# Kernel optimization log

Hardware: AMD Instinct MI355X
Metric: run time of the kernel (lower is better)

## Reference

```python
import jax, jax.numpy as jnp
import numpy as np

AUX_LOSS_COEFF = 0.03125  # config.aux_loss_coeff


def setup_inputs() -> dict:
    key = jax.random.key(0)
    k0, k1 = jax.random.split(key, 2)
    B, T, d, m = 2, 2048, 2048, 16384
    activations = jax.random.normal(k0, (B, T, d), dtype=jnp.float32)
    # kaiming-uniform-ish init, then unit-norm rows (as in _initialize_weights)
    W_enc = jax.random.normal(k1, (m, d), dtype=jnp.float32)
    W_enc = W_enc / (jnp.linalg.norm(W_enc, axis=1, keepdims=True) + 1e-8)
    b_enc = jnp.zeros((m,), dtype=jnp.float32)
    W_emb = W_enc.T  # tied init: W_emb.weight = W_enc.weight.T, shape [d, m]
    steps_since_active = jnp.zeros((m,), dtype=jnp.int32)  # buffer, starts at 0
    return {
        "activations": activations,
        "W_enc": W_enc,
        "b_enc": b_enc,
        "W_emb": W_emb,
        "steps_since_active": steps_since_active,
        "topk": 64,
        "dead_window": 1000,
    }


def reference(activations, W_enc, b_enc, W_emb, steps_since_active, topk, dead_window):
    B, T, d = activations.shape
    m = W_enc.shape[0]
    # pre_act = W_enc(activations)  -> [B, T, m]
    pre_act = jnp.einsum("btd,md->btm", activations, W_enc) + b_enc
    # top-k over concept dim
    top_vals, top_idx = jax.lax.top_k(pre_act, topk)  # [B, T, k]
    # sparse = zeros scatter top_vals at top_idx along last dim
    flat_idx = top_idx.reshape(-1, topk)   # [B*T, k]
    flat_vals = top_vals.reshape(-1, topk)
    rows = jnp.arange(flat_idx.shape[0])[:, None]
    sparse = (
        jnp.zeros((flat_idx.shape[0], m), dtype=pre_act.dtype)
        .at[rows, flat_idx]
        .set(flat_vals)
        .reshape(B, T, m)
    )
    # encoded = W_emb(sparse) -> [B, T, d]
    encoded = jnp.einsum("btm,dm->btd", sparse, W_emb)
    # aux loss on dead concepts (dead_mask all False at init -> 0.0)
    dead_mask = (steps_since_active >= dead_window).astype(pre_act.dtype)  # [m]
    n_dead = jnp.sum(dead_mask)
    denom = jnp.maximum(n_dead * B * T, 1.0)
    dead_mean = jnp.sum(pre_act * dead_mask) / denom
    aux_loss = jnp.where(n_dead > 0, -dead_mean * AUX_LOSS_COEFF, jnp.zeros((), pre_act.dtype))
    return encoded, aux_loss
```

## Files before the change

kernel.cpp:

```cpp
#include <hip/hip_runtime.h>
#include <cfloat>
#include <climits>


typedef __attribute__((ext_vector_type(8))) short short8;
typedef __attribute__((ext_vector_type(4))) float f32x4;

#define NC      96
#define KFIN    64
#define TAU     1e-3f
#define AUXC    0.03125f
#define MCONC   16384
#define DDIM    2048
#define CAP     768

__device__ __forceinline__ ushort f2bf(float f) {
  unsigned u = __float_as_uint(f);
  u += 0x7fff + ((u >> 16) & 1);
  return (ushort)(u >> 16);
}
__device__ __forceinline__ float bf2f(ushort h) {
  return __uint_as_float(((unsigned)h) << 16);
}

__global__ void k_init(float* dead_sum, int* n_dead, int* wl_count) {
  *dead_sum = 0.f;
  *n_dead = 0;
  *wl_count = 0;
}

__global__ void k_count_dead(const int* __restrict__ steps, const int* __restrict__ dw,
                             int m, int* __restrict__ n_dead) {
  int i = blockIdx.x * blockDim.x + threadIdx.x;
  if (i < m && steps[i] >= *dw) atomicAdd(n_dead, 1);
}

__global__ void k_final(const float* __restrict__ ds, const int* __restrict__ nd,
                        float* __restrict__ outp, float BT) {
  int n = *nd;
  float denom = fmaxf((float)n * BT, 1.0f);
  outp[0] = (n > 0) ? -((*ds) / denom) * AUXC : 0.0f;
}

__global__ __launch_bounds__(256)
void k_stage2(const float* __restrict__ srcA, ushort* __restrict__ dstA, int totA,
              const float* __restrict__ srcB, ushort* __restrict__ dstB, int totB,
              int K) {
  int idx = blockIdx.x * 256 + threadIdx.x;
  const float* src;
  ushort* dst;
  int t;
  if (idx < totA) { src = srcA; dst = dstA; t = idx; }
  else if (idx < totA + totB) { src = srcB; dst = dstB; t = idx - totA; }
  else return;
  int nch = K >> 5;
  int row = t / nch, c = t - row * nch;
  const float* s = src + (size_t)row * K + c * 32;
  float f[32];
#pragma unroll
  for (int q = 0; q < 8; ++q) *(float4*)&f[q * 4] = *(const float4*)(s + q * 4);
  ushort hi[32];
  float lof[32];
#pragma unroll
  for (int e = 0; e < 32; ++e) {
    hi[e] = f2bf(f[e]);
    lof[e] = f[e] - bf2f(hi[e]);
  }
  ushort* d = dst + (size_t)row * ((size_t)K * 2) + c * 64;
#pragma unroll
  for (int q = 0; q < 4; ++q) {
    short8 o;
#pragma unroll
    for (int e = 0; e < 8; ++e) o[e] = (short)hi[q * 8 + e];
    *(short8*)(d + q * 8) = o;
  }
#pragma unroll
  for (int q = 0; q < 4; ++q) {
    short8 o;
#pragma unroll
    for (int e = 0; e < 8; ++e) o[e] = (short)f2bf(lof[q * 8 + e]);
    *(short8*)(d + 32 + q * 8) = o;
  }
}

__device__ __forceinline__ void gload16(const void* g, void* l) {
  __builtin_amdgcn_global_load_lds((const __attribute__((address_space(1))) void*)g,
                                   (__attribute__((address_space(3))) void*)l, 16, 0, 0);
}

__global__ __launch_bounds__(256, 3)
void k_gemm3(const ushort* __restrict__ Ast, const ushort* __restrict__ Bst,
             const float* __restrict__ bias, float* __restrict__ C,
             int row0, int K, int m, int nbm) {
  __shared__ ushort As[128 * 64];
  __shared__ ushort Bs[128 * 64];
  const int tid = threadIdx.x;
  const int lane = tid & 63, w = tid >> 6;
  const int wm = w >> 1, wn = w & 1;

  const int nbn = m >> 7;
  const int nwg = nbm * nbn;
  const int q = nwg >> 3, r = nwg & 7;
  const int x = blockIdx.x & 7, i0 = blockIdx.x >> 3;
  const int wg = (x < r) ? x * (q + 1) + i0 : r * (q + 1) + (x - r) * q + i0;
  const int bm = wg / nbn, bn = wg % nbn;

  const size_t K2 = (size_t)K * 2;
  const int nch = K >> 5;

  const int gr = lane >> 3;
  const int swz = (((lane & 7) ^ gr) << 3);
  const size_t arow0 = (size_t)(row0 + bm * 128);
  const size_t brow0 = (size_t)(bn * 128);

  f32x4 acc[4][4];
#pragma unroll
  for (int i = 0; i < 4; ++i)
#pragma unroll
    for (int j = 0; j < 4; ++j) acc[i][j] = (f32x4)(0.f);

  const int kg = lane >> 4;
  const int j7 = lane & 7;
  const int sh = ((kg ^ j7) << 3);
  const int rbase = (lane & 15) * 64;

  for (int c = 0; c < nch; ++c) {
#pragma unroll
    for (int t = 0; t < 4; ++t) {
      int i = w * 4 + t;
      int rr = i * 8 + gr;
      gload16(Ast + (arow0 + rr) * K2 + (size_t)c * 64 + swz, (void*)(As + i * 512));
      gload16(Bst + (brow0 + rr) * K2 + (size_t)c * 64 + swz, (void*)(Bs + i * 512));
    }
    __syncthreads();
    short8 ah[4], al[4], bh[4], bl[4];
#pragma unroll
    for (int f = 0; f < 4; ++f) {
      const ushort* pa = As + (wm * 64 + f * 16) * 64 + rbase;
      ah[f] = *(const short8*)(pa + sh);
      al[f] = *(const short8*)(pa + (sh ^ 32));
      const ushort* pb = Bs + (wn * 64 + f * 16) * 64 + rbase;
      bh[f] = *(const short8*)(pb + sh);
      bl[f] = *(const short8*)(pb + (sh ^ 32));
    }
#pragma unroll
    for (int fm = 0; fm < 4; ++fm)
#pragma unroll
      for (int fn = 0; fn < 4; ++fn) {
        acc[fm][fn] = __builtin_amdgcn_mfma_f32_16x16x32_bf16(ah[fm], bh[fn], acc[fm][fn], 0, 0, 0);
        acc[fm][fn] = __builtin_amdgcn_mfma_f32_16x16x32_bf16(ah[fm], bl[fn], acc[fm][fn], 0, 0, 0);
        acc[fm][fn] = __builtin_amdgcn_mfma_f32_16x16x32_bf16(al[fm], bh[fn], acc[fm][fn], 0, 0, 0);
      }
    __syncthreads();
  }

  const int orow = bm * 128 + wm * 64;
  const int ocol = bn * 128 + wn * 64;
#pragma unroll
  for (int fn = 0; fn < 4; ++fn) {
    float bb = bias[ocol + fn * 16 + (lane & 15)];
#pragma unroll
    for (int fm = 0; fm < 4; ++fm) {
      int rb = orow + fm * 16 + (lane >> 4) * 4;
#pragma unroll
      for (int rr = 0; rr < 4; ++rr)
        __builtin_nontemporal_store(acc[fm][fn][rr] + bb,
            &C[(size_t)(rb + rr) * m + ocol + fn * 16 + (lane & 15)]);
    }
  }
}

__global__ __launch_bounds__(256)
void k_topk(const float* __restrict__ preact, int row0,
            const int* __restrict__ steps, const int* __restrict__ dw,
            const int* __restrict__ topk_d,
            float* __restrict__ cvals, int* __restrict__ cidx,
            float* __restrict__ dead_sum,
            int* __restrict__ rowflag, int* __restrict__ wl, int* __restrict__ wl_count,
            float* __restrict__ tvals, int* __restrict__ tidx) {
  __shared__ float dred[4];
  __shared__ float wmx[4], wmn[4];
  __shared__ int scnt;
  __shared__ int pos;
  __shared__ float cval_s[CAP];
  __shared__ int cidx_s[CAP];
  __shared__ float vk1_s, vk_s;
  __shared__ int flag_s;
  const int tid = threadIdx.x;
  const int lane = tid & 63;
  const int grow = row0 + blockIdx.x;
  const float* pr = preact + (size_t)blockIdx.x * MCONC;

  int kt = *topk_d;
  if (kt > KFIN) kt = KFIN;
  if (kt < 1) kt = 1;

  float v[64];
#pragma unroll
  for (int c = 0; c < 16; ++c) {
    const f32x4* p4 = (const f32x4*)(pr + (size_t)c * 1024 + tid * 4);
    f32x4 t4 = __builtin_nontemporal_load(p4);
    v[c * 4 + 0] = t4[0]; v[c * 4 + 1] = t4[1];
    v[c * 4 + 2] = t4[2]; v[c * 4 + 3] = t4[3];
  }

  int dwv = *dw;
  float ds = 0.f;
#pragma unroll
  for (int c = 0; c < 16; ++c) {
    int4 st = *(const int4*)(steps + c * 1024 + tid * 4);
    if (st.x >= dwv) ds += v[c * 4 + 0];
    if (st.y >= dwv) ds += v[c * 4 + 1];
    if (st.z >= dwv) ds += v[c * 4 + 2];
    if (st.w >= dwv) ds += v[c * 4 + 3];
  }
  for (int off = 32; off; off >>= 1) ds += __shfl_down(ds, off);
  if (lane == 0) dred[tid >> 6] = ds;

  float mx = -FLT_MAX, mn = FLT_MAX;
#pragma unroll
  for (int i = 0; i < 64; ++i) { mx = fmaxf(mx, v[i]); mn = fminf(mn, v[i]); }
  for (int off = 32; off; off >>= 1) {
    mx = fmaxf(mx, __shfl_xor(mx, off));
    mn = fminf(mn, __shfl_xor(mn, off));
  }
  if (lane == 0) { wmx[tid >> 6] = mx; wmn[tid >> 6] = mn; }
  __syncthreads();
  if (tid == 0) {
    float t = dred[0] + dred[1] + dred[2] + dred[3];
    if (t != 0.f) atomicAdd(dead_sum, t);
  }
  float row_mx = fmaxf(fmaxf(wmx[0], wmx[1]), fmaxf(wmx[2], wmx[3]));
  float row_mn = fminf(fminf(wmn[0], wmn[1]), fminf(wmn[2], wmn[3]));

  float lo = row_mn - 1.0f, hi = row_mx;
  float t = lo;
  bool found = false;
  for (int it = 0; it < 22 && !found; ++it) {
    float mid = 0.5f * (lo + hi);
    __syncthreads();
    if (tid == 0) scnt = 0;
    __syncthreads();
    int cl = 0;
#pragma unroll
    for (int i = 0; i < 64; ++i) cl += (v[i] > mid);
    for (int off = 32; off; off >>= 1) cl += __shfl_xor(cl, off);
    if (lane == 0) atomicAdd(&scnt, cl);
    __syncthreads();
    int cnt = scnt;
    if (cnt >= NC && cnt <= CAP) { t = mid; found = true; }
    else if (cnt < NC) hi = mid;
    else lo = mid;
  }
  if (!found) t = lo;

  __syncthreads();
  if (tid == 0) pos = 0;
  __syncthreads();
#pragma unroll
  for (int i = 0; i < 64; ++i) {
    if (v[i] > t) {
      int p = atomicAdd(&pos, 1);
      if (p < CAP) {
        cval_s[p] = v[i];
        cidx_s[p] = ((i >> 2) << 10) | (tid << 2) | (i & 3);
      }
    }
  }
  __syncthreads();
  int Cn = pos < CAP ? pos : CAP;

  int rnk[3];
  float mvv[3];
  int mii[3];
#pragma unroll
  for (int jj = 0; jj < 3; ++jj) {
    int j = tid + jj * 256;
    rnk[jj] = INT_MAX;
    if (j < Cn) {
      float my = cval_s[j];
      int myidx = cidx_s[j];
      int rank = 0;
      for (int c = 0; c < Cn; ++c) {
        float o = cval_s[c];
        rank += (o > my) || (o == my && cidx_s[c] < myidx);
      }
      rnk[jj] = rank; mvv[jj] = my; mii[jj] = myidx;
      if (rank < NC) {
        cvals[(size_t)grow * NC + rank] = my;
        cidx[(size_t)grow * NC + rank] = myidx;
      }
      if (rank == kt - 1) vk1_s = my;
      if (rank == kt)     vk_s  = my;
    }
  }
  __syncthreads();
  if (tid == 0) {
    int f = (vk1_s - vk_s < TAU) ? 1 : 0;
    rowflag[grow] = f;
    flag_s = f;
    if (f) { int p = atomicAdd(wl_count, 1); wl[p] = grow; }
  }
  __syncthreads();
  if (!flag_s) {
#pragma unroll
    for (int jj = 0; jj < 3; ++jj) {
      if (rnk[jj] < kt) {
        tvals[(size_t)grow * KFIN + rnk[jj]] = mvv[jj];
        tidx[(size_t)grow * KFIN + rnk[jj]] = mii[jj];
      }
    }
  }
}

__global__ __launch_bounds__(256)
void k_dots(const int* __restrict__ wl, const int* __restrict__ wl_count,
            const int* __restrict__ cidx, const float* __restrict__ act,
            const float* __restrict__ Wenc, const float* __restrict__ bias,
            double* __restrict__ dv, int d) {
  __shared__ float arow[DDIM];
  const int b = blockIdx.x;
  if (b >= (*wl_count) * 8) return;
  const int row = wl[b >> 3], part = b & 7;
  for (int i = threadIdx.x; i < d; i += 256) arow[i] = act[(size_t)row * d + i];
  __syncthreads();
  const int lane = threadIdx.x & 63, w = threadIdx.x >> 6;
#pragma unroll
  for (int cc = 0; cc < 3; ++cc) {
    int c = part * 12 + w * 3 + cc;
    int ci = cidx[(size_t)row * NC + c];
    const float* wrow = Wenc + (size_t)ci * d;
    double s = 0.0;
    for (int i = lane; i < d; i += 64)
      s += (double)arow[i] * (double)wrow[i];
    for (int off = 32; off; off >>= 1) s += __shfl_down(s, off);
    if (lane == 0) dv[(size_t)row * NC + c] = s + (double)bias[ci];
  }
}

__global__ __launch_bounds__(128)
void k_select(const float* __restrict__ cvals, const int* __restrict__ cidx,
              const int* __restrict__ rowflag, const double* __restrict__ dv,
              const int* __restrict__ topk_d,
              float* __restrict__ tvals, int* __restrict__ tidx) {
  const int row = blockIdx.x, tid = threadIdx.x;
  if (!rowflag[row]) return;
  int kt = *topk_d;
  if (kt > KFIN) kt = KFIN;
  if (kt < 1) kt = 1;
  __shared__ double sdv[NC];
  if (tid < NC) sdv[tid] = dv[(size_t)row * NC + tid];
  __syncthreads();
  if (tid < NC) {
    double my = sdv[tid];
    int rank = 0;
#pragma unroll 8
    for (int c = 0; c < NC; ++c) {
      double v = sdv[c];
      rank += (v > my) || (v == my && c < tid);
    }
    if (rank < kt) {
      tvals[(size_t)row * KFIN + rank] = cvals[(size_t)row * NC + tid];
      tidx[(size_t)row * KFIN + rank] = cidx[(size_t)row * NC + tid];
    }
  }
}

__global__ __launch_bounds__(256)
void k_transpose(const float* __restrict__ src, ushort* __restrict__ dst, int d, int m) {
  __shared__ float tile[32][33];
  int mb = blockIdx.x * 32, db = blockIdx.y * 32;
  int tx = threadIdx.x, ty = threadIdx.y;
#pragma unroll
  for (int i = 0; i < 32; i += 8)
    tile[ty + i][tx] = src[(size_t)(db + ty + i) * m + mb + tx];
  __syncthreads();
#pragma unroll
  for (int i = 0; i < 32; i += 8)
    dst[(size_t)(mb + ty + i) * d + db + tx] = f2bf(tile[tx][ty + i]);
}

__global__ __launch_bounds__(256)
void k_decode_t(const float* __restrict__ tvals, const int* __restrict__ tidx,
                const int* __restrict__ topk_d, const ushort* __restrict__ Wt,
                float* __restrict__ out, int d) {
  __shared__ float sv[KFIN];
  __shared__ int si[KFIN];
  const int row = blockIdx.x, tid = threadIdx.x;
  int kt = *topk_d;
  if (kt > KFIN) kt = KFIN;
  if (tid < kt) {
    sv[tid] = tvals[(size_t)row * KFIN + tid];
    si[tid] = tidx[(size_t)row * KFIN + tid];
  }
  __syncthreads();
  for (int base = tid * 8; base < d; base += 2048) {
    float a0 = 0, a1 = 0, a2 = 0, a3 = 0, a4 = 0, a5 = 0, a6 = 0, a7 = 0;
#pragma unroll 4
    for (int j = 0; j < kt; ++j) {
      float vv = sv[j];
      short8 wv = *(const short8*)(Wt + (size_t)si[j] * d + base);
      a0 = fmaf(vv, bf2f((ushort)wv[0]), a0);
      a1 = fmaf(vv, bf2f((ushort)wv[1]), a1);
      a2 = fmaf(vv, bf2f((ushort)wv[2]), a2);
      a3 = fmaf(vv, bf2f((ushort)wv[3]), a3);
      a4 = fmaf(vv, bf2f((ushort)wv[4]), a4);
      a5 = fmaf(vv, bf2f((ushort)wv[5]), a5);
      a6 = fmaf(vv, bf2f((ushort)wv[6]), a6);
      a7 = fmaf(vv, bf2f((ushort)wv[7]), a7);
    }
    float* o = out + (size_t)row * d + base;
    *(float4*)o = make_float4(a0, a1, a2, a3);
    *(float4*)(o + 4) = make_float4(a4, a5, a6, a7);
  }
}

__global__ __launch_bounds__(256)
void k_decode_g(const float* __restrict__ tvals, const int* __restrict__ tidx,
                const int* __restrict__ topk_d, const float* __restrict__ Wemb,
                float* __restrict__ out, int d, int m) {
  __shared__ float sv[KFIN];
  __shared__ int si[KFIN];
  const int row = blockIdx.x, tid = threadIdx.x;
  int kt = *topk_d;
  if (kt > KFIN) kt = KFIN;
  if (tid < kt) {
    sv[tid] = tvals[(size_t)row * KFIN + tid];
    si[tid] = tidx[(size_t)row * KFIN + tid];
  }
  __syncthreads();
  for (int base = tid * 8; base < d; base += 2048) {
    float acc[8] = {0, 0, 0, 0, 0, 0, 0, 0};
    for (int j = 0; j < kt; ++j) {
      float vv = sv[j];
      int ix = si[j];
#pragma unroll
      for (int e = 0; e < 8; ++e)
        acc[e] = fmaf(vv, Wemb[(size_t)(base + e) * m + ix], acc[e]);
    }
    float* o = out + (size_t)row * d + base;
    *(float4*)o = *(float4*)&acc[0];
    *(float4*)(o + 4) = *(float4*)&acc[4];
  }
}

extern "C" void kernel_launch(void* const* d_in, const int* in_sizes, int n_in,
                              void* d_out, int out_size, void* d_ws, size_t ws_size,
                              hipStream_t stream) {
  const float* act   = (const float*)d_in[0];
  const float* Wenc  = (const float*)d_in[1];
  const float* benc  = (const float*)d_in[2];
  const float* Wemb  = (const float*)d_in[3];
  const int*   steps = (const int*)d_in[4];
  const int*   topk  = (const int*)d_in[5];
  const int*   dwin  = (const int*)d_in[6];
  const int m = in_sizes[2];
  const int d = in_sizes[1] / m;
  const int rows = in_sizes[0] / d;
  float* out = (float*)d_out;

  char* ws = (char*)d_ws;
  float* dead_sum = (float*)ws;
  int*   n_dead   = (int*)(ws + 8);
  int*   wl_count = (int*)(ws + 16);
  size_t off = 256;
  float* cvals = (float*)(ws + off); off += (size_t)rows * NC * 4;
  int*   cidx  = (int*)(ws + off);   off += (size_t)rows * NC * 4;
  float* tvals = (float*)(ws + off); off += (size_t)rows * KFIN * 4;
  int*   tidx  = (int*)(ws + off);   off += (size_t)rows * KFIN * 4;
  int*   rowflag = (int*)(ws + off); off += (size_t)rows * 4;
  int*   wl      = (int*)(ws + off); off += (size_t)rows * 4;
  double* dv     = (double*)(ws + off); off += (size_t)rows * NC * 8;
  ushort* Ast  = (ushort*)(ws + off); off += (size_t)rows * d * 4;
  ushort* Bst  = (ushort*)(ws + off); off += (size_t)m * d * 4;

  const size_t wembT_bytes = (size_t)m * d * sizeof(ushort);
  const size_t row_bytes = (size_t)m * sizeof(float);
  size_t avail = (ws_size > off) ? ws_size - off : 0;

  ushort* WembT = nullptr;
  if (avail >= wembT_bytes + 128 * row_bytes) {
    WembT = (ushort*)(ws + off);
    off += wembT_bytes;
    avail -= wembT_bytes;
  }
  int chunk = (int)(avail / row_bytes);
  if (chunk > rows) chunk = rows;
  chunk &= ~127;
  if (chunk < 128) chunk = 128;
  float* preact = (float*)(ws + off);

  k_init<<<1, 1, 0, stream>>>(dead_sum, n_dead, wl_count);
  k_count_dead<<<(m + 255) / 256, 256, 0, stream>>>(steps, dwin, m, n_dead);

  int totA = rows * (d >> 5);
  int totB = m * (d >> 5);
  k_stage2<<<(totA + totB + 255) / 256, 256, 0, stream>>>(act, Ast, totA, Wenc, Bst, totB, d);

  for (int r0 = 0; r0 < rows; r0 += chunk) {
    int cr = rows - r0;
    if (cr > chunk) cr = chunk;
    int nbm = cr / 128;
    int nwg = nbm * (m / 128);
    k_gemm3<<<nwg, 256, 0, stream>>>(Ast, Bst, benc, preact, r0, d, m, nbm);
    k_topk<<<cr, 256, 0, stream>>>(preact, r0, steps, dwin, topk,
                                   cvals, cidx, dead_sum,
                                   rowflag, wl, wl_count, tvals, tidx);
  }

  k_dots<<<rows * 8, 256, 0, stream>>>(wl, wl_count, cidx, act, Wenc, benc, dv, d);
  k_select<<<rows, 128, 0, stream>>>(cvals, cidx, rowflag, dv, topk, tvals, tidx);

  if (WembT) {
    dim3 gt(m / 32, d / 32);
    k_transpose<<<gt, dim3(32, 8), 0, stream>>>(Wemb, WembT, d, m);
    k_decode_t<<<rows, 256, 0, stream>>>(tvals, tidx, topk, WembT, out, d);
  } else {
    k_decode_g<<<rows, 256, 0, stream>>>(tvals, tidx, topk, Wemb, out, d, m);
  }

  k_final<<<1, 1, 0, stream>>>(dead_sum, n_dead, out + (size_t)rows * d, (float)rows);
}
```

Baseline: 1.315 ms.

## Fuse W_emb transpose into prep kernel, seed top-k threshold search, grid-stride dots

The W_emb transpose/bf16 conversion now runs as extra blocks of the split-bf16 staging kernel, so there is one launch instead of two and the two memory-bound jobs can overlap. The top-k threshold bisection now starts from mean + 2*stddev of the row instead of the midpoint of the min/max range. This aims to land in the candidate count window in fewer block-wide count passes, at the cost of also accumulating sum and sum of squares. The dead-row dots kernel becomes grid-stride with one block per row instead of eight, which cuts the many early-exit blocks but reduces parallelism when many rows need refinement.

```diff
diff --git a/kernel.cpp b/kernel.cpp
--- a/kernel.cpp
+++ b/kernel.cpp
@@ -43,44 +43,62 @@
 }
 
 __global__ __launch_bounds__(256)
-void k_stage2(const float* __restrict__ srcA, ushort* __restrict__ dstA, int totA,
-              const float* __restrict__ srcB, ushort* __restrict__ dstB, int totB,
-              int K) {
-  int idx = blockIdx.x * 256 + threadIdx.x;
-  const float* src;
-  ushort* dst;
-  int t;
-  if (idx < totA) { src = srcA; dst = dstA; t = idx; }
-  else if (idx < totA + totB) { src = srcB; dst = dstB; t = idx - totA; }
-  else return;
-  int nch = K >> 5;
-  int row = t / nch, c = t - row * nch;
-  const float* s = src + (size_t)row * K + c * 32;
-  float f[32];
-#pragma unroll
-  for (int q = 0; q < 8; ++q) *(float4*)&f[q * 4] = *(const float4*)(s + q * 4);
-  ushort hi[32];
-  float lof[32];
-#pragma unroll
-  for (int e = 0; e < 32; ++e) {
-    hi[e] = f2bf(f[e]);
-    lof[e] = f[e] - bf2f(hi[e]);
-  }
-  ushort* d = dst + (size_t)row * ((size_t)K * 2) + c * 64;
-#pragma unroll
-  for (int q = 0; q < 4; ++q) {
-    short8 o;
-#pragma unroll
-    for (int e = 0; e < 8; ++e) o[e] = (short)hi[q * 8 + e];
-    *(short8*)(d + q * 8) = o;
-  }
-#pragma unroll
-  for (int q = 0; q < 4; ++q) {
-    short8 o;
-#pragma unroll
-    for (int e = 0; e < 8; ++e) o[e] = (short)f2bf(lof[q * 8 + e]);
-    *(short8*)(d + 32 + q * 8) = o;
-  }
+void k_prep(const float* __restrict__ srcA, ushort* __restrict__ dstA, int totA,
+            const float* __restrict__ srcB, ushort* __restrict__ dstB, int totB,
+            int K,
+            const float* __restrict__ Wemb, ushort* __restrict__ WembT,
+            int d, int m, int nstage) {
+  __shared__ float tile[32][33];
+  const int b = blockIdx.x;
+  if (b < nstage) {
+    int idx = b * 256 + threadIdx.x;
+    const float* src;
+    ushort* dst;
+    int t;
+    if (idx < totA) { src = srcA; dst = dstA; t = idx; }
+    else if (idx < totA + totB) { src = srcB; dst = dstB; t = idx - totA; }
+    else return;
+    int nch = K >> 5;
+    int row = t / nch, c = t - row * nch;
+    const float* s = src + (size_t)row * K + c * 32;
+    float f[32];
+#pragma unroll
+    for (int q = 0; q < 8; ++q) *(float4*)&f[q * 4] = *(const float4*)(s + q * 4);
+    ushort hi[32];
+    float lof[32];
+#pragma unroll
+    for (int e = 0; e < 32; ++e) {
+      hi[e] = f2bf(f[e]);
+      lof[e] = f[e] - bf2f(hi[e]);
+    }
+    ushort* dd = dst + (size_t)row * ((size_t)K * 2) + c * 64;
+#pragma unroll
+    for (int q = 0; q < 4; ++q) {
+      short8 o;
+#pragma unroll
+      for (int e = 0; e < 8; ++e) o[e] = (short)hi[q * 8 + e];
+      *(short8*)(dd + q * 8) = o;
+    }
+#pragma unroll
+    for (int q = 0; q < 4; ++q) {
+      short8 o;
+#pragma unroll
+      for (int e = 0; e < 8; ++e) o[e] = (short)f2bf(lof[q * 8 + e]);
+      *(short8*)(dd + 32 + q * 8) = o;
+    }
+    return;
+  }
+  const int tb = b - nstage;
+  const int nmb = m >> 5;
+  const int mb = (tb % nmb) * 32, db = (tb / nmb) * 32;
+  const int tx = threadIdx.x & 31, ty = threadIdx.x >> 5;
+#pragma unroll
+  for (int i = 0; i < 32; i += 8)
+    tile[ty + i][tx] = Wemb[(size_t)(db + ty + i) * m + mb + tx];
+  __syncthreads();
+#pragma unroll
+  for (int i = 0; i < 32; i += 8)
+    WembT[(size_t)(mb + ty + i) * d + db + tx] = f2bf(tile[tx][ty + i]);
 }
 
 __device__ __forceinline__ void gload16(const void* g, void* l) {
@@ -180,6 +198,7 @@
             float* __restrict__ tvals, int* __restrict__ tidx) {
   __shared__ float dred[4];
   __shared__ float wmx[4], wmn[4];
+  __shared__ float sm1[4], sm2[4];
   __shared__ int scnt;
   __shared__ int pos;
   __shared__ float cval_s[CAP];
@@ -217,14 +236,19 @@
   for (int off = 32; off; off >>= 1) ds += __shfl_down(ds, off);
   if (lane == 0) dred[tid >> 6] = ds;
 
-  float mx = -FLT_MAX, mn = FLT_MAX;
-#pragma unroll
-  for (int i = 0; i < 64; ++i) { mx = fmaxf(mx, v[i]); mn = fminf(mn, v[i]); }
+  float mx = -FLT_MAX, mn = FLT_MAX, s1 = 0.f, s2 = 0.f;
+#pragma unroll
+  for (int i = 0; i < 64; ++i) {
+    mx = fmaxf(mx, v[i]); mn = fminf(mn, v[i]);
+    s1 += v[i]; s2 = fmaf(v[i], v[i], s2);
+  }
   for (int off = 32; off; off >>= 1) {
     mx = fmaxf(mx, __shfl_xor(mx, off));
     mn = fminf(mn, __shfl_xor(mn, off));
-  }
-  if (lane == 0) { wmx[tid >> 6] = mx; wmn[tid >> 6] = mn; }
+    s1 += __shfl_xor(s1, off);
+    s2 += __shfl_xor(s2, off);
+  }
+  if (lane == 0) { wmx[tid >> 6] = mx; wmn[tid >> 6] = mn; sm1[tid >> 6] = s1; sm2[tid >> 6] = s2; }
   __syncthreads();
   if (tid == 0) {
     float t = dred[0] + dred[1] + dred[2] + dred[3];
@@ -232,12 +256,16 @@
   }
   float row_mx = fmaxf(fmaxf(wmx[0], wmx[1]), fmaxf(wmx[2], wmx[3]));
   float row_mn = fminf(fminf(wmn[0], wmn[1]), fminf(wmn[2], wmn[3]));
+  float T1 = sm1[0] + sm1[1] + sm1[2] + sm1[3];
+  float T2 = sm2[0] + sm2[1] + sm2[2] + sm2[3];
+  float mu = T1 * (1.f / 16384.f);
+  float var = fmaxf(T2 * (1.f / 16384.f) - mu * mu, 0.f);
+  float mid = mu + 2.0f * sqrtf(var);
 
   float lo = row_mn - 1.0f, hi = row_mx;
   float t = lo;
   bool found = false;
-  for (int it = 0; it < 22 && !found; ++it) {
-    float mid = 0.5f * (lo + hi);
+  for (int it = 0; it < 23 && !found; ++it) {
     __syncthreads();
     if (tid == 0) scnt = 0;
     __syncthreads();
@@ -251,6 +279,7 @@
     if (cnt >= NC && cnt <= CAP) { t = mid; found = true; }
     else if (cnt < NC) hi = mid;
     else lo = mid;
+    mid = 0.5f * (lo + hi);
   }
   if (!found) t = lo;
 
@@ -319,22 +348,24 @@
             const float* __restrict__ Wenc, const float* __restrict__ bias,
             double* __restrict__ dv, int d) {
   __shared__ float arow[DDIM];
-  const int b = blockIdx.x;
-  if (b >= (*wl_count) * 8) return;
-  const int row = wl[b >> 3], part = b & 7;
-  for (int i = threadIdx.x; i < d; i += 256) arow[i] = act[(size_t)row * d + i];
-  __syncthreads();
+  const int total = (*wl_count) * 8;
   const int lane = threadIdx.x & 63, w = threadIdx.x >> 6;
-#pragma unroll
-  for (int cc = 0; cc < 3; ++cc) {
-    int c = part * 12 + w * 3 + cc;
-    int ci = cidx[(size_t)row * NC + c];
-    const float* wrow = Wenc + (size_t)ci * d;
-    double s = 0.0;
-    for (int i = lane; i < d; i += 64)
-      s += (double)arow[i] * (double)wrow[i];
-    for (int off = 32; off; off >>= 1) s += __shfl_down(s, off);
-    if (lane == 0) dv[(size_t)row * NC + c] = s + (double)bias[ci];
+  for (int b = blockIdx.x; b < total; b += gridDim.x) {
+    const int row = wl[b >> 3], part = b & 7;
+    __syncthreads();
+    for (int i = threadIdx.x; i < d; i += 256) arow[i] = act[(size_t)row * d + i];
+    __syncthreads();
+#pragma unroll
+    for (int cc = 0; cc < 3; ++cc) {
+      int c = part * 12 + w * 3 + cc;
+      int ci = cidx[(size_t)row * NC + c];
+      const float* wrow = Wenc + (size_t)ci * d;
+      double s = 0.0;
+      for (int i = lane; i < d; i += 64)
+        s += (double)arow[i] * (double)wrow[i];
+      for (int off = 32; off; off >>= 1) s += __shfl_down(s, off);
+      if (lane == 0) dv[(size_t)row * NC + c] = s + (double)bias[ci];
+    }
   }
 }
 
@@ -364,20 +395,6 @@
       tidx[(size_t)row * KFIN + rank] = cidx[(size_t)row * NC + tid];
     }
   }
-}
-
-__global__ __launch_bounds__(256)
-void k_transpose(const float* __restrict__ src, ushort* __restrict__ dst, int d, int m) {
-  __shared__ float tile[32][33];
-  int mb = blockIdx.x * 32, db = blockIdx.y * 32;
-  int tx = threadIdx.x, ty = threadIdx.y;
-#pragma unroll
-  for (int i = 0; i < 32; i += 8)
-    tile[ty + i][tx] = src[(size_t)(db + ty + i) * m + mb + tx];
-  __syncthreads();
-#pragma unroll
-  for (int i = 0; i < 32; i += 8)
-    dst[(size_t)(mb + ty + i) * d + db + tx] = f2bf(tile[tx][ty + i]);
 }
 
 __global__ __launch_bounds__(256)
@@ -495,7 +512,10 @@
 
   int totA = rows * (d >> 5);
   int totB = m * (d >> 5);
-  k_stage2<<<(totA + totB + 255) / 256, 256, 0, stream>>>(act, Ast, totA, Wenc, Bst, totB, d);
+  int nstage = (totA + totB + 255) / 256;
+  int ntrans = WembT ? (m / 32) * (d / 32) : 0;
+  k_prep<<<nstage + ntrans, 256, 0, stream>>>(act, Ast, totA, Wenc, Bst, totB, d,
+                                              Wemb, WembT, d, m, nstage);
 
   for (int r0 = 0; r0 < rows; r0 += chunk) {
     int cr = rows - r0;
@@ -508,12 +528,10 @@
                                    rowflag, wl, wl_count, tvals, tidx);
   }
 
-  k_dots<<<rows * 8, 256, 0, stream>>>(wl, wl_count, cidx, act, Wenc, benc, dv, d);
+  k_dots<<<rows, 256, 0, stream>>>(wl, wl_count, cidx, act, Wenc, benc, dv, d);
   k_select<<<rows, 128, 0, stream>>>(cvals, cidx, rowflag, dv, topk, tvals, tidx);
 
   if (WembT) {
-    dim3 gt(m / 32, d / 32);
-    k_transpose<<<gt, dim3(32, 8), 0, stream>>>(Wemb, WembT, d, m);
     k_decode_t<<<rows, 256, 0, stream>>>(tvals, tidx, topk, WembT, out, d);
   } else {
     k_decode_g<<<rows, 256, 0, stream>>>(tvals, tidx, topk, Wemb, out, d, m);
```

Measured after the change: 1.256 ms. -4.5%, faster.
